# Optimization experiments

Measured on AMD Instinct MI355X. Metric: run time of the kernel, lower is better.

Reference implementation:

```python
import jax, jax.numpy as jnp
import numpy as np

BN_EPS = 1e-5
DIST_EPS = 1e-8


def setup_inputs() -> dict:
    key = jax.random.key(0)
    ks = jax.random.split(key, 10)
    B, Ni, Mi = 4, 16384, 4096
    C1, C2 = 64, 64
    Cin = C1 + C2  # 128, mlp=[128,128,128]
    inp = {
        "unknown": jax.random.normal(ks[0], (B * Ni, 3), dtype=jnp.float32),
        "unknown_batch_cnt": np.full(B, Ni, dtype=np.int64),
        "known": jax.random.normal(ks[1], (B * Mi, 3), dtype=jnp.float32),
        "known_batch_cnt": np.full(B, Mi, dtype=np.int64),
        "unknown_feats": jax.random.normal(ks[2], (B * Ni, C1), dtype=jnp.float32),
        "known_feats": jax.random.normal(ks[3], (B * Mi, C2), dtype=jnp.float32),
        "W1": jax.random.normal(ks[4], (128, Cin), dtype=jnp.float32) * 0.05,
        "g1": jnp.ones((128,), dtype=jnp.float32),
        "b1": jnp.zeros((128,), dtype=jnp.float32),
        "W2": jax.random.normal(ks[5], (128, 128), dtype=jnp.float32) * 0.05,
        "g2": jnp.ones((128,), dtype=jnp.float32),
        "b2": jnp.zeros((128,), dtype=jnp.float32),
    }
    return inp


def _three_nn(u, k):
    # u: (B,Ni,3), k: (B,Mi,3) -> dist (B,Ni,3), idx (B,Ni,3) within each batch
    d2 = (jnp.sum(u * u, -1)[:, :, None] + jnp.sum(k * k, -1)[:, None, :]
          - 2.0 * jnp.einsum("bnd,bmd->bnm", u, k))  # (B,Ni,Mi)
    neg_d2, idx = jax.lax.top_k(-d2, 3)
    dist = jnp.sqrt(jnp.maximum(-neg_d2, 0.0))
    return dist, idx


def _bn_relu(y, g, b):
    # BatchNorm2d over the point dim (training-mode batch stats), then ReLU
    mu = jnp.mean(y, axis=0)
    var = jnp.mean((y - mu) ** 2, axis=0)
    return jax.nn.relu((y - mu) * jax.lax.rsqrt(var + BN_EPS) * g + b)


def reference(unknown, unknown_batch_cnt, known, known_batch_cnt,
              unknown_feats, known_feats, W1, g1, b1, W2, g2, b2):
    ucnt = np.asarray(unknown_batch_cnt)
    kcnt = np.asarray(known_batch_cnt)
    B = ucnt.shape[0]
    Ni, Mi = int(ucnt[0]), int(kcnt[0])  # equal-count ragged batches
    C2 = known_feats.shape[1]

    u = unknown.reshape(B, Ni, 3)
    k = known.reshape(B, Mi, 3)
    dist, idx = _three_nn(u, k)

    dist_recip = 1.0 / (dist + DIST_EPS)
    weight = dist_recip / jnp.sum(dist_recip, axis=-1, keepdims=True)  # (B,Ni,3)

    kf = known_feats.reshape(B, Mi, C2)
    gathered = kf[jnp.arange(B)[:, None, None], idx]  # (B,Ni,3,C2)
    interp = jnp.sum(weight[..., None] * gathered, axis=2).reshape(B * Ni, C2)

    x = jnp.concatenate([interp, unknown_feats], axis=1)  # (N, C2+C1)
    x = _bn_relu(x @ W1.T, g1, b1)
    x = _bn_relu(x @ W2.T, g2, b2)
    return x
```

## Files before the change

### kernel.cpp

```cpp
#include <hip/hip_runtime.h>
#include <hip/hip_bf16.h>

#define GRID  32
#define NCELL (GRID * GRID * GRID)
#define H     0.3125f
#define INVH  3.2f
#define OFF   5.0f
#define SUBW  8
#define XPAD  136
#define NREP  16

using f32x4  = __attribute__((ext_vector_type(4))) float;
using bf16x8 = __attribute__((ext_vector_type(8))) short;

static __device__ inline short f2bs(float f) {
  __hip_bfloat16 h = __float2bfloat16(f);
  return __builtin_bit_cast(short, h);
}
static __device__ inline float bs2f(short s) {
  return __bfloat162float(__builtin_bit_cast(__hip_bfloat16, s));
}
static __device__ inline int cellco(float x) {
  int c = (int)((x + OFF) * INVH);
  return min(GRID - 1, max(0, c));
}

#define INSF(dv, mv)                                   \
  {                                                    \
    bool q0 = dv < b0, q1 = dv < b1, q2 = dv < b2;     \
    float P0 = b0, P1 = b1; int Q0 = j0, Q1 = j1;      \
    b2 = q1 ? P1 : (q2 ? dv : b2);                     \
    j2 = q1 ? Q1 : (q2 ? mv : j2);                     \
    b1 = q0 ? P0 : (q1 ? dv : P1);                     \
    j1 = q0 ? Q0 : (q1 ? mv : Q1);                     \
    b0 = q0 ? dv : P0;                                 \
    j0 = q0 ? mv : Q0;                                 \
  }

#define MERGE3(lo_mk, hi_mk)                                                        \
  for (int mk = lo_mk; mk <= hi_mk; mk <<= 1) {                                     \
    float ob0 = __shfl_xor(b0, mk), ob1 = __shfl_xor(b1, mk), ob2 = __shfl_xor(b2, mk); \
    int   oj0 = __shfl_xor(j0, mk), oj1 = __shfl_xor(j1, mk), oj2 = __shfl_xor(j2, mk); \
    INSF(ob0, oj0); INSF(ob1, oj1); INSF(ob2, oj2);                                 \
  }

__global__ __launch_bounds__(256) void zero_k(int4* __restrict__ dst, int n4) {
  int i = blockIdx.x * 256 + threadIdx.x;
  if (i < n4) dst[i] = int4{0, 0, 0, 0};
}

__global__ __launch_bounds__(256) void hist_k(
    const float* __restrict__ known, int Mtot, int Mi,
    const float* __restrict__ unknown, int Ntot,
    int* __restrict__ khist, int* __restrict__ qhist,
    int* __restrict__ kcell, int* __restrict__ qcell,
    const float* __restrict__ W1, const float* __restrict__ W2,
    __hip_bfloat16* __restrict__ Wb1, __hip_bfloat16* __restrict__ Wb2) {
  int i = blockIdx.x * 256 + threadIdx.x;
  if (i < 128 * 128) {
    Wb1[i] = __float2bfloat16(W1[i]);
    Wb2[i] = __float2bfloat16(W2[i]);
  }
  if (i < Mtot) {
    int b = i / Mi;
    float x = known[(size_t)i * 3], y = known[(size_t)i * 3 + 1], z = known[(size_t)i * 3 + 2];
    int c = b * NCELL + (cellco(z) * GRID + cellco(y)) * GRID + cellco(x);
    kcell[i] = c;
    atomicAdd(&khist[c], 1);
  }
  if (i < Ntot) {
    int Ni = Ntot / (Mtot / Mi);
    int b = i / Ni;
    float x = unknown[(size_t)i * 3], y = unknown[(size_t)i * 3 + 1], z = unknown[(size_t)i * 3 + 2];
    int c = b * NCELL + (cellco(z) * GRID + cellco(y)) * GRID + cellco(x);
    qcell[i] = c;
    atomicAdd(&qhist[c], 1);
  }
}

__global__ __launch_bounds__(256) void scan1_k(
    const int4* __restrict__ Hc4, int* __restrict__ bsum) {
  __shared__ int sh[256];
  int t = threadIdx.x;
  int4 h = Hc4[blockIdx.x * 256 + t];
  int s = h.x + h.y + h.z + h.w;
  sh[t] = s;
  __syncthreads();
  for (int d = 128; d > 0; d >>= 1) {
    if (t < d) sh[t] += sh[t + d];
    __syncthreads();
  }
  if (t == 0) bsum[blockIdx.x] = sh[0];
}

__global__ __launch_bounds__(256) void scan2_k(
    int* __restrict__ bsum, int nb, int* __restrict__ kstart, int* __restrict__ qstart,
    int nc, int Mtot, int Ntot) {
  __shared__ int sh[256];
  int t = threadIdx.x;
  int v = (t < nb) ? bsum[t] : 0;
  sh[t] = v;
  __syncthreads();
  for (int d = 1; d < 256; d <<= 1) {
    int u = (t >= d) ? sh[t - d] : 0;
    __syncthreads();
    sh[t] += u;
    __syncthreads();
  }
  if (t < nb) bsum[t] = sh[t] - v;
  if (t == 0) { kstart[nc] = Mtot; qstart[nc] = Ntot; }
}

__global__ __launch_bounds__(256) void scan3_k(
    const int4* __restrict__ Hc4, const int* __restrict__ bsum,
    int* __restrict__ kstart, int* __restrict__ kfill,
    int* __restrict__ qstart, int* __restrict__ qfill, int nc, int Mtot) {
  __shared__ int sh[256];
  int t = threadIdx.x;
  int g4 = blockIdx.x * 256 + t;
  int4 h = Hc4[g4];
  int s = h.x + h.y + h.z + h.w;
  sh[t] = s;
  __syncthreads();
  for (int d = 1; d < 256; d <<= 1) {
    int u = (t >= d) ? sh[t - d] : 0;
    __syncthreads();
    sh[t] += u;
    __syncthreads();
  }
  int run = bsum[blockIdx.x] + sh[t] - s;
  int hv[4] = {h.x, h.y, h.z, h.w};
#pragma unroll
  for (int j = 0; j < 4; ++j) {
    int g = g4 * 4 + j;
    if (g < nc) { kstart[g] = run; kfill[g] = run; }
    else        { int q = g - nc; qstart[q] = run - Mtot; qfill[q] = run - Mtot; }
    run += hv[j];
  }
}

__global__ __launch_bounds__(256) void scatter_k(
    const float* __restrict__ known, int Mtot, int Mi,
    const float* __restrict__ unknown, int Ntot,
    const int* __restrict__ kcell, const int* __restrict__ qcell,
    int* __restrict__ kfill, int* __restrict__ qfill,
    f32x4* __restrict__ k4s, int* __restrict__ korder,
    f32x4* __restrict__ u4s, int* __restrict__ qorder) {
  int i = blockIdx.x * 256 + threadIdx.x;
  if (i < Mtot) {
    int slot = atomicAdd(&kfill[kcell[i]], 1);
    float x = known[(size_t)i * 3], y = known[(size_t)i * 3 + 1], z = known[(size_t)i * 3 + 2];
    f32x4 v;
    v[0] = -2.f * x; v[1] = -2.f * y; v[2] = -2.f * z;
    v[3] = x * x + y * y + z * z;
    k4s[slot] = v;
    korder[slot] = i - (i / Mi) * Mi;
  }
  if (i < Ntot) {
    int slot = atomicAdd(&qfill[qcell[i]], 1);
    float x = unknown[(size_t)i * 3], y = unknown[(size_t)i * 3 + 1], z = unknown[(size_t)i * 3 + 2];
    f32x4 v;
    v[0] = x; v[1] = y; v[2] = z;
    v[3] = __fmaf_rn(x, x, __fmaf_rn(y, y, z * z));
    u4s[slot] = v;
    qorder[slot] = i;
  }
}

static __device__ __forceinline__ void scan_box_strided(
    int R, int sub, int stride, int cx, int cy, int cz, int cellbase,
    const int* __restrict__ cstart, const f32x4* __restrict__ k4s,
    const int* __restrict__ korder,
    float ux, float uy, float uz,
    float& b0, float& b1, float& b2, int& j0, int& j1, int& j2) {
  int zlo = max(cz - R, 0), zhi = min(cz + R, GRID - 1);
  int ylo = max(cy - R, 0), yhi = min(cy + R, GRID - 1);
  int xlo = max(cx - R, 0), xhi = min(cx + R, GRID - 1);
  int ny = yhi - ylo + 1;
  int nrows = (zhi - zlo + 1) * ny;
  for (int rid = sub; rid < nrows; rid += stride) {
    int zz = rid / ny;
    int y  = ylo + (rid - zz * ny);
    int row = cellbase + ((zlo + zz) * GRID + y) * GRID;
    int s = cstart[row + xlo];
    int e = cstart[row + xhi + 1];
    for (int i = s; i < e; ++i) {
      f32x4 k = k4s[i];
      float d = __fmaf_rn(ux, k[0], __fmaf_rn(uy, k[1], __fmaf_rn(uz, k[2], k[3])));
      int m = korder[i];
      INSF(d, m);
    }
  }
}

__global__ __launch_bounds__(256) void knn_grid_k(
    const f32x4* __restrict__ u4s, const int* __restrict__ qorder,
    const int* __restrict__ cstart, const f32x4* __restrict__ k4s,
    const int* __restrict__ korder, int Ni,
    float* __restrict__ w, int* __restrict__ idx,
    int* __restrict__ rcnt, int* __restrict__ rlist, float* __restrict__ rd3) {
  int nwc = gridDim.x * 4;
  int gw  = blockIdx.x * 4 + (threadIdx.x >> 6);
  int wchunk = (gw * 997) & (nwc - 1);
  int s   = wchunk * 8 + ((threadIdx.x & 63) / SUBW);
  int sub = threadIdx.x & (SUBW - 1);
  f32x4 u4 = u4s[s];
  int p = qorder[s];
  int b = p / Ni;
  float ux = u4[0], uy = u4[1], uz = u4[2], uu = u4[3];
  int cx = cellco(ux), cy = cellco(uy), cz = cellco(uz);
  int cellbase = b * NCELL;
  int xlo = max(cx - 1, 0), xhi = min(cx + 1, GRID - 1);

  float b0 = 3e38f, b1 = 3e38f, b2 = 3e38f;
  int   j0 = 0,     j1 = 0,     j2 = 0;
#pragma unroll
  for (int dz = -1; dz <= 1; ++dz) {
    int z = cz + dz;
    if (z < 0 || z >= GRID) continue;
#pragma unroll
    for (int dy = -1; dy <= 1; ++dy) {
      int y = cy + dy;
      if (y < 0 || y >= GRID) continue;
      int row = cellbase + (z * GRID + y) * GRID;
      int cs = cstart[row + xlo];
      int ce = cstart[row + xhi + 1];
      for (int i = cs + sub; i < ce; i += SUBW) {
        f32x4 k = k4s[i];
        float d = __fmaf_rn(ux, k[0], __fmaf_rn(uy, k[1], __fmaf_rn(uz, k[2], k[3])));
        int m = korder[i];
        INSF(d, m);
      }
    }
  }
  MERGE3(1, SUBW / 2);

  float d3sq = b2 + uu;
  bool ok = d3sq <= H * H;

  if (sub == 0) {
    if (ok) {
      float d0 = sqrtf(fmaxf(b0 + uu, 0.f));
      float d1 = sqrtf(fmaxf(b1 + uu, 0.f));
      float d2 = sqrtf(fmaxf(b2 + uu, 0.f));
      float r0 = 1.f / (d0 + 1e-8f);
      float r1 = 1.f / (d1 + 1e-8f);
      float r2 = 1.f / (d2 + 1e-8f);
      float rs = 1.f / (r0 + r1 + r2);
      size_t o = (size_t)p * 3;
      w[o] = r0 * rs; w[o + 1] = r1 * rs; w[o + 2] = r2 * rs;
      idx[o] = j0; idx[o + 1] = j1; idx[o + 2] = j2;
    } else {
      int t = atomicAdd(rcnt, 1);
      rlist[t] = s;
      rd3[t] = d3sq;
    }
  }
}

__global__ __launch_bounds__(256) void knn_retry_k(
    const f32x4* __restrict__ u4s, const int* __restrict__ qorder,
    const int* __restrict__ rlist, const float* __restrict__ rd3,
    const int* __restrict__ rcnt,
    const int* __restrict__ cstart, const f32x4* __restrict__ k4s,
    const int* __restrict__ korder, int Ni,
    float* __restrict__ w, int* __restrict__ idx) {
  int lane = threadIdx.x & 63;
  int wv   = blockIdx.x * 4 + (threadIdx.x >> 6);
  int nw   = gridDim.x * 4;
  int cnt  = rcnt[0];
  for (int q = wv; q < cnt; q += nw) {
    int sq = rlist[q];
    f32x4 u4 = u4s[sq];
    int p = qorder[sq];
    int b = p / Ni;
    float ux = u4[0], uy = u4[1], uz = u4[2], uu = u4[3];
    int cx = cellco(ux), cy = cellco(uy), cz = cellco(uz);
    int cellbase = b * NCELL;

    float d3sq = rd3[q];
    int Rc = 1;
    float b0, b1, b2; int j0, j1, j2;
    bool ok = false;
    while (!ok) {
      if (d3sq < 1e30f) {
        Rc = max((int)ceilf(sqrtf(fmaxf(d3sq, 0.f)) * INVH), Rc + 1);
      } else {
        Rc = Rc * 2;
      }
      Rc = min(Rc, GRID);
      b0 = b1 = b2 = 3e38f; j0 = j1 = j2 = 0;
      scan_box_strided(Rc, lane, 64, cx, cy, cz, cellbase, cstart, k4s, korder,
                       ux, uy, uz, b0, b1, b2, j0, j1, j2);
      MERGE3(1, 32);
      d3sq = b2 + uu;
      float cov = (float)Rc * H;
      ok = (d3sq <= cov * cov) || (Rc >= GRID);
    }
    if (lane == 0) {
      float d0 = sqrtf(fmaxf(b0 + uu, 0.f));
      float d1 = sqrtf(fmaxf(b1 + uu, 0.f));
      float d2 = sqrtf(fmaxf(b2 + uu, 0.f));
      float r0 = 1.f / (d0 + 1e-8f);
      float r1 = 1.f / (d1 + 1e-8f);
      float r2 = 1.f / (d2 + 1e-8f);
      float rs = 1.f / (r0 + r1 + r2);
      size_t o = (size_t)p * 3;
      w[o] = r0 * rs; w[o + 1] = r1 * rs; w[o + 2] = r2 * rs;
      idx[o] = j0; idx[o + 1] = j1; idx[o + 2] = j2;
    }
  }
}

template <bool F32OUT>
static __device__ __forceinline__ void gemm_half(
    const short* xs, const short* Ws, int row0,
    float* yf, __hip_bfloat16* yb, float* ls, float* lq) {
  int t = threadIdx.x;
  int lane = t & 63;
  int wv = t >> 6;
  int r = lane & 15, g = lane >> 4;
  int tile = wv >> 1, half = wv & 1;
  int trow = tile * 16;

  bf16x8 a[4];
#pragma unroll
  for (int q = 0; q < 4; ++q)
    a[q] = *reinterpret_cast<const bf16x8*>(&xs[(trow + r) * XPAD + g * 8 + q * 32]);

  int orow = row0 + trow + g * 4;
#pragma unroll
  for (int ct = 0; ct < 4; ++ct) {
    int ocol = half * 64 + ct * 16 + r;
    f32x4 acc = {0.f, 0.f, 0.f, 0.f};
    size_t bbase = (size_t)ocol * 128 + g * 8;
#pragma unroll
    for (int q = 0; q < 4; ++q) {
      bf16x8 bfr = *reinterpret_cast<const bf16x8*>(Ws + bbase + q * 32);
      acc = __builtin_amdgcn_mfma_f32_16x16x32_bf16(a[q], bfr, acc, 0, 0, 0);
    }
    if (F32OUT) {
#pragma unroll
      for (int i = 0; i < 4; ++i)
        yf[(size_t)(orow + i) * 128 + ocol] = acc[i];
    } else {
#pragma unroll
      for (int i = 0; i < 4; ++i)
        yb[(size_t)(orow + i) * 128 + ocol] = __float2bfloat16(acc[i]);
    }
    float s  = acc[0] + acc[1] + acc[2] + acc[3];
    float q2 = acc[0] * acc[0] + acc[1] * acc[1] + acc[2] * acc[2] + acc[3] * acc[3];
    s  += __shfl_xor(s, 16);  s  += __shfl_xor(s, 32);
    q2 += __shfl_xor(q2, 16); q2 += __shfl_xor(q2, 32);
    if (g == 0) {
      atomicAdd(&ls[ocol], s);
      atomicAdd(&lq[ocol], q2);
    }
  }
}

__global__ __launch_bounds__(256) void gemm1_fused_k(
    const float* __restrict__ kf, const float* __restrict__ uf,
    const float* __restrict__ wgt, const int* __restrict__ idx,
    const __hip_bfloat16* __restrict__ Wb, __hip_bfloat16* __restrict__ Yb,
    float* __restrict__ stats, int Ni, int Mi) {
  __shared__ short xs[32 * XPAD];
  __shared__ float ls[128], lq[128];
  int t = threadIdx.x;
  if (t < 128) { ls[t] = 0.f; lq[t] = 0.f; }
  int row0 = blockIdx.x * 32;

  int rr = t >> 3, c0 = (t & 7) * 16;
  int p = row0 + rr;
  short tmp[16];
  if (c0 < 64) {
    size_t o = (size_t)p * 3;
    float w0 = wgt[o], w1 = wgt[o + 1], w2 = wgt[o + 2];
    int i0 = idx[o], i1 = idx[o + 1], i2 = idx[o + 2];
    int b = p / Ni;
    const float* kfb = kf + (size_t)b * Mi * 64 + c0;
    const f32x4* r0p = reinterpret_cast<const f32x4*>(kfb + (size_t)i0 * 64);
    const f32x4* r1p = reinterpret_cast<const f32x4*>(kfb + (size_t)i1 * 64);
    const f32x4* r2p = reinterpret_cast<const f32x4*>(kfb + (size_t)i2 * 64);
#pragma unroll
    for (int j = 0; j < 4; ++j) {
      f32x4 av = r0p[j], bv = r1p[j], cv = r2p[j];
#pragma unroll
      for (int e = 0; e < 4; ++e)
        tmp[j * 4 + e] = f2bs(w0 * av[e] + w1 * bv[e] + w2 * cv[e]);
    }
  } else {
    const f32x4* ufp = reinterpret_cast<const f32x4*>(uf + (size_t)p * 64 + (c0 - 64));
#pragma unroll
    for (int j = 0; j < 4; ++j) {
      f32x4 av = ufp[j];
#pragma unroll
      for (int e = 0; e < 4; ++e)
        tmp[j * 4 + e] = f2bs(av[e]);
    }
  }
  *reinterpret_cast<bf16x8*>(&xs[rr * XPAD + c0])     = *reinterpret_cast<bf16x8*>(&tmp[0]);
  *reinterpret_cast<bf16x8*>(&xs[rr * XPAD + c0 + 8]) = *reinterpret_cast<bf16x8*>(&tmp[8]);
  __syncthreads();

  gemm_half<false>(xs, reinterpret_cast<const short*>(Wb), row0, nullptr, Yb, ls, lq);

  __syncthreads();
  if (t < 128) {
    int rep = blockIdx.x & (NREP - 1);
    atomicAdd(&stats[rep * 256 + t], ls[t]);
    atomicAdd(&stats[rep * 256 + 128 + t], lq[t]);
  }
}

__global__ __launch_bounds__(256) void gemm2_bn_k(
    const __hip_bfloat16* __restrict__ Y1, const float* __restrict__ AB,
    const __hip_bfloat16* __restrict__ Wb, float* __restrict__ Yf,
    float* __restrict__ stats) {
  __shared__ short xs[32 * XPAD];
  __shared__ float ls[128], lq[128];
  int t = threadIdx.x;
  if (t < 128) { ls[t] = 0.f; lq[t] = 0.f; }
  int row0 = blockIdx.x * 32;

  int rr = t >> 3, c0 = (t & 7) * 16;
  int p = row0 + rr;
  const short* Ys = reinterpret_cast<const short*>(Y1);
  bf16x8 v0 = *reinterpret_cast<const bf16x8*>(Ys + (size_t)p * 128 + c0);
  bf16x8 v1 = *reinterpret_cast<const bf16x8*>(Ys + (size_t)p * 128 + c0 + 8);
  short tmp[16];
#pragma unroll
  for (int j = 0; j < 8; ++j)
    tmp[j] = f2bs(fmaxf(bs2f(v0[j]) * AB[c0 + j] + AB[128 + c0 + j], 0.f));
#pragma unroll
  for (int j = 0; j < 8; ++j)
    tmp[8 + j] = f2bs(fmaxf(bs2f(v1[j]) * AB[c0 + 8 + j] + AB[128 + c0 + 8 + j], 0.f));
  *reinterpret_cast<bf16x8*>(&xs[rr * XPAD + c0])     = *reinterpret_cast<bf16x8*>(&tmp[0]);
  *reinterpret_cast<bf16x8*>(&xs[rr * XPAD + c0 + 8]) = *reinterpret_cast<bf16x8*>(&tmp[8]);
  __syncthreads();

  gemm_half<true>(xs, reinterpret_cast<const short*>(Wb), row0, Yf, nullptr, ls, lq);

  __syncthreads();
  if (t < 128) {
    int rep = blockIdx.x & (NREP - 1);
    atomicAdd(&stats[rep * 256 + t], ls[t]);
    atomicAdd(&stats[rep * 256 + 128 + t], lq[t]);
  }
}

__global__ void finalize_k(const float* __restrict__ stats, const float* __restrict__ g,
                           const float* __restrict__ bb, float invN, float* __restrict__ AB) {
  int c = threadIdx.x;
  float s = 0.f, q = 0.f;
  for (int rpl = 0; rpl < NREP; ++rpl) {
    s += stats[rpl * 256 + c];
    q += stats[rpl * 256 + 128 + c];
  }
  float mu  = s * invN;
  float var = q * invN - mu * mu;
  float A = rsqrtf(var + 1e-5f) * g[c];
  AB[c] = A;
  AB[128 + c] = bb[c] - mu * A;
}

__global__ __launch_bounds__(256) void bnrelu_f32_k(
    float* __restrict__ Y, const float* __restrict__ AB, long n4) {
  long i = (long)blockIdx.x * 256 + threadIdx.x;
  long stride = (long)gridDim.x * 256;
  for (; i < n4; i += stride) {
    f32x4 y = reinterpret_cast<f32x4*>(Y)[i];
    int c0 = (int)((i * 4) & 127);
    f32x4 A  = *reinterpret_cast<const f32x4*>(AB + c0);
    f32x4 Bv = *reinterpret_cast<const f32x4*>(AB + 128 + c0);
    f32x4 o;
#pragma unroll
    for (int j = 0; j < 4; ++j) o[j] = fmaxf(y[j] * A[j] + Bv[j], 0.f);
    reinterpret_cast<f32x4*>(Y)[i] = o;
  }
}

extern "C" void kernel_launch(void* const* d_in, const int* in_sizes, int n_in,
                              void* d_out, int out_size, void* d_ws, size_t ws_size,
                              hipStream_t stream) {
  const float* unknown = (const float*)d_in[0];
  const float* known   = (const float*)d_in[2];
  const float* uf      = (const float*)d_in[4];
  const float* kf      = (const float*)d_in[5];
  const float* W1      = (const float*)d_in[6];
  const float* g1      = (const float*)d_in[7];
  const float* b1      = (const float*)d_in[8];
  const float* W2      = (const float*)d_in[9];
  const float* g2      = (const float*)d_in[10];
  const float* b2      = (const float*)d_in[11];

  int B    = in_sizes[1];
  int Ntot = in_sizes[0] / 3;
  int Mtot = in_sizes[2] / 3;
  int Ni = Ntot / B, Mi = Mtot / B;
  int nc = B * NCELL;
  int n2 = 2 * nc;

  char* ws = (char*)d_ws;
  size_t off = 0;
  auto alloc = [&](size_t bytes) {
    void* p = ws + off;
    off += (bytes + 255) & ~(size_t)255;
    return p;
  };
  float* stats  = (float*)alloc(2 * NREP * 256 * 4);
  int*   rcnt   = (int*)alloc(4);
  int*   khist  = (int*)alloc((size_t)n2 * 4);
  int*   qhist  = khist + nc;
  size_t zero_bytes = (size_t)((char*)(khist + n2) - (char*)stats);
  int*   kstart = (int*)alloc((size_t)(nc + 1) * 4);
  int*   qstart = (int*)alloc((size_t)(nc + 1) * 4);
  int*   kfill  = (int*)alloc((size_t)nc * 4);
  int*   qfill  = (int*)alloc((size_t)nc * 4);
  int*   kcell  = (int*)alloc((size_t)Mtot * 4);
  int*   qcell  = (int*)alloc((size_t)Ntot * 4);
  int*   korder = (int*)alloc((size_t)Mtot * 4);
  int*   qorder = (int*)alloc((size_t)Ntot * 4);
  int*   bsum   = (int*)alloc((size_t)(n2 / 1024) * 4);
  int*   rlist  = (int*)alloc((size_t)Ntot * 4);
  float* rd3    = (float*)alloc((size_t)Ntot * 4);
  f32x4* k4s    = (f32x4*)alloc((size_t)Mtot * 16);
  f32x4* u4s    = (f32x4*)alloc((size_t)Ntot * 16);
  float* wgt    = (float*)alloc((size_t)Ntot * 3 * 4);
  int*   idx    = (int*)alloc((size_t)Ntot * 3 * 4);
  __hip_bfloat16* y1b = (__hip_bfloat16*)alloc((size_t)Ntot * 128 * 2);
  __hip_bfloat16* Wb1 = (__hip_bfloat16*)alloc(128 * 128 * 2);
  __hip_bfloat16* Wb2 = (__hip_bfloat16*)alloc(128 * 128 * 2);
  float* AB1 = (float*)alloc(256 * 4);
  float* AB2 = (float*)alloc(256 * 4);

  float* y2 = (float*)d_out;
  long n4 = (long)Ntot * 128 / 4;
  float invN = 1.0f / (float)Ntot;
  int nb = n2 / 1024;
  float* stats2 = stats + NREP * 256;
  int zn4 = (int)(zero_bytes / 16);

  zero_k<<<(zn4 + 255) / 256, 256, 0, stream>>>((int4*)stats, zn4);
  hist_k<<<(Ntot + 255) / 256, 256, 0, stream>>>(known, Mtot, Mi, unknown, Ntot,
                                                 khist, qhist, kcell, qcell, W1, W2, Wb1, Wb2);
  scan1_k<<<nb, 256, 0, stream>>>((const int4*)khist, bsum);
  scan2_k<<<1, 256, 0, stream>>>(bsum, nb, kstart, qstart, nc, Mtot, Ntot);
  scan3_k<<<nb, 256, 0, stream>>>((const int4*)khist, bsum, kstart, kfill, qstart, qfill, nc, Mtot);
  scatter_k<<<(Ntot + 255) / 256, 256, 0, stream>>>(known, Mtot, Mi, unknown, Ntot,
                                                    kcell, qcell, kfill, qfill, k4s, korder, u4s, qorder);
  knn_grid_k<<<Ntot / 32, 256, 0, stream>>>(u4s, qorder, kstart, k4s, korder, Ni,
                                            wgt, idx, rcnt, rlist, rd3);
  knn_retry_k<<<1024, 256, 0, stream>>>(u4s, qorder, rlist, rd3, rcnt,
                                        kstart, k4s, korder, Ni, wgt, idx);
  gemm1_fused_k<<<Ntot / 32, 256, 0, stream>>>(kf, uf, wgt, idx, Wb1, y1b, stats, Ni, Mi);
  finalize_k<<<1, 128, 0, stream>>>(stats, g1, b1, invN, AB1);
  gemm2_bn_k<<<Ntot / 32, 256, 0, stream>>>(y1b, AB1, Wb2, y2, stats2);
  finalize_k<<<1, 128, 0, stream>>>(stats2, g2, b2, invN, AB2);
  bnrelu_f32_k<<<2048, 256, 0, stream>>>(y2, AB2, n4);
}
```

Baseline: 161.4 us.

## Fuse both MLP layers and BN passes into one persistent kernel with grid barriers

New measurement: 394.6 us. +144.5%, slower.

```diff
diff --git a/kernel.cpp b/kernel.cpp
--- a/kernel.cpp
+++ b/kernel.cpp
@@ -16,9 +16,6 @@
 static __device__ inline short f2bs(float f) {
   __hip_bfloat16 h = __float2bfloat16(f);
   return __builtin_bit_cast(short, h);
-}
-static __device__ inline float bs2f(short s) {
-  return __bfloat162float(__builtin_bit_cast(__hip_bfloat16, s));
 }
 static __device__ inline int cellco(float x) {
   int c = (int)((x + OFF) * INVH);
@@ -312,44 +309,56 @@
   }
 }
 
-template <bool F32OUT>
-static __device__ __forceinline__ void gemm_half(
-    const short* xs, const short* Ws, int row0,
-    float* yf, __hip_bfloat16* yb, float* ls, float* lq) {
-  int t = threadIdx.x;
-  int lane = t & 63;
-  int wv = t >> 6;
-  int r = lane & 15, g = lane >> 4;
-  int tile = wv >> 1, half = wv & 1;
-  int trow = tile * 16;
-
+
+static __device__ __forceinline__ void grid_bar(int* bar, int target) {
+  __syncthreads();
+  if (threadIdx.x == 0) {
+    __threadfence();
+    __hip_atomic_fetch_add(bar, 1, __ATOMIC_ACQ_REL, __HIP_MEMORY_SCOPE_AGENT);
+    while (__hip_atomic_load(bar, __ATOMIC_ACQUIRE, __HIP_MEMORY_SCOPE_AGENT) < target) {}
+  }
+  __syncthreads();
+}
+
+#define TGEOM                                  \
+  int t = threadIdx.x;                         \
+  int lane = t & 63;                           \
+  int wv = t >> 6;                             \
+  int r = lane & 15, g = lane >> 4;            \
+  int wtile = wv >> 1, half = wv & 1;          \
+  int trow = wtile * 16;
+
+static __device__ __forceinline__ void gemm_tile(
+    const short* xs, const short* Ws, f32x4 acc[4]) {
+  TGEOM
+  (void)wtile;
   bf16x8 a[4];
 #pragma unroll
   for (int q = 0; q < 4; ++q)
     a[q] = *reinterpret_cast<const bf16x8*>(&xs[(trow + r) * XPAD + g * 8 + q * 32]);
-
-  int orow = row0 + trow + g * 4;
 #pragma unroll
   for (int ct = 0; ct < 4; ++ct) {
     int ocol = half * 64 + ct * 16 + r;
-    f32x4 acc = {0.f, 0.f, 0.f, 0.f};
+    f32x4 v = {0.f, 0.f, 0.f, 0.f};
     size_t bbase = (size_t)ocol * 128 + g * 8;
 #pragma unroll
     for (int q = 0; q < 4; ++q) {
       bf16x8 bfr = *reinterpret_cast<const bf16x8*>(Ws + bbase + q * 32);
-      acc = __builtin_amdgcn_mfma_f32_16x16x32_bf16(a[q], bfr, acc, 0, 0, 0);
-    }
-    if (F32OUT) {
-#pragma unroll
-      for (int i = 0; i < 4; ++i)
-        yf[(size_t)(orow + i) * 128 + ocol] = acc[i];
-    } else {
-#pragma unroll
-      for (int i = 0; i < 4; ++i)
-        yb[(size_t)(orow + i) * 128 + ocol] = __float2bfloat16(acc[i]);
-    }
-    float s  = acc[0] + acc[1] + acc[2] + acc[3];
-    float q2 = acc[0] * acc[0] + acc[1] * acc[1] + acc[2] * acc[2] + acc[3] * acc[3];
+      v = __builtin_amdgcn_mfma_f32_16x16x32_bf16(a[q], bfr, v, 0, 0, 0);
+    }
+    acc[ct] = v;
+  }
+}
+
+static __device__ __forceinline__ void acc_stats(const f32x4 acc[4], float* ls, float* lq) {
+  TGEOM
+  (void)wtile; (void)trow;
+#pragma unroll
+  for (int ct = 0; ct < 4; ++ct) {
+    int ocol = half * 64 + ct * 16 + r;
+    float s  = acc[ct][0] + acc[ct][1] + acc[ct][2] + acc[ct][3];
+    float q2 = acc[ct][0] * acc[ct][0] + acc[ct][1] * acc[ct][1]
+             + acc[ct][2] * acc[ct][2] + acc[ct][3] * acc[ct][3];
     s  += __shfl_xor(s, 16);  s  += __shfl_xor(s, 32);
     q2 += __shfl_xor(q2, 16); q2 += __shfl_xor(q2, 32);
     if (g == 0) {
@@ -359,124 +368,142 @@
   }
 }
 
-__global__ __launch_bounds__(256) void gemm1_fused_k(
+__global__ __launch_bounds__(256, 4) void mlp_fused_k(
     const float* __restrict__ kf, const float* __restrict__ uf,
     const float* __restrict__ wgt, const int* __restrict__ idx,
-    const __hip_bfloat16* __restrict__ Wb, __hip_bfloat16* __restrict__ Yb,
-    float* __restrict__ stats, int Ni, int Mi) {
+    const __hip_bfloat16* __restrict__ Wb1, const __hip_bfloat16* __restrict__ Wb2,
+    const float* __restrict__ g1, const float* __restrict__ b1v,
+    const float* __restrict__ g2, const float* __restrict__ b2v,
+    float* __restrict__ stats, int* __restrict__ bar,
+    float* __restrict__ y2, int Ni, int Mi, float invN, int nblocks) {
   __shared__ short xs[32 * XPAD];
   __shared__ float ls[128], lq[128];
-  int t = threadIdx.x;
+  __shared__ float ABs[256];
+  TGEOM
+  const short* W1s = reinterpret_cast<const short*>(Wb1);
+  const short* W2s = reinterpret_cast<const short*>(Wb2);
+  float* stats2 = stats + NREP * 256;
+  int rep = blockIdx.x & (NREP - 1);
+  int srow = t >> 3, c0 = (t & 7) * 16;
+
   if (t < 128) { ls[t] = 0.f; lq[t] = 0.f; }
-  int row0 = blockIdx.x * 32;
-
-  int rr = t >> 3, c0 = (t & 7) * 16;
-  int p = row0 + rr;
-  short tmp[16];
-  if (c0 < 64) {
-    size_t o = (size_t)p * 3;
-    float w0 = wgt[o], w1 = wgt[o + 1], w2 = wgt[o + 2];
-    int i0 = idx[o], i1 = idx[o + 1], i2 = idx[o + 2];
-    int b = p / Ni;
-    const float* kfb = kf + (size_t)b * Mi * 64 + c0;
-    const f32x4* r0p = reinterpret_cast<const f32x4*>(kfb + (size_t)i0 * 64);
-    const f32x4* r1p = reinterpret_cast<const f32x4*>(kfb + (size_t)i1 * 64);
-    const f32x4* r2p = reinterpret_cast<const f32x4*>(kfb + (size_t)i2 * 64);
-#pragma unroll
-    for (int j = 0; j < 4; ++j) {
-      f32x4 av = r0p[j], bv = r1p[j], cv = r2p[j];
-#pragma unroll
-      for (int e = 0; e < 4; ++e)
-        tmp[j * 4 + e] = f2bs(w0 * av[e] + w1 * bv[e] + w2 * cv[e]);
-    }
-  } else {
-    const f32x4* ufp = reinterpret_cast<const f32x4*>(uf + (size_t)p * 64 + (c0 - 64));
-#pragma unroll
-    for (int j = 0; j < 4; ++j) {
-      f32x4 av = ufp[j];
-#pragma unroll
-      for (int e = 0; e < 4; ++e)
-        tmp[j * 4 + e] = f2bs(av[e]);
-    }
-  }
-  *reinterpret_cast<bf16x8*>(&xs[rr * XPAD + c0])     = *reinterpret_cast<bf16x8*>(&tmp[0]);
-  *reinterpret_cast<bf16x8*>(&xs[rr * XPAD + c0 + 8]) = *reinterpret_cast<bf16x8*>(&tmp[8]);
-  __syncthreads();
-
-  gemm_half<false>(xs, reinterpret_cast<const short*>(Wb), row0, nullptr, Yb, ls, lq);
-
-  __syncthreads();
+  __syncthreads();
+
+  f32x4 acc1[2][4];
+#pragma unroll 2
+  for (int tt = 0; tt < 2; ++tt) {
+    int row0 = (blockIdx.x * 2 + tt) * 32;
+    int p = row0 + srow;
+    short tmp[16];
+    if (c0 < 64) {
+      size_t o = (size_t)p * 3;
+      float w0 = wgt[o], w1 = wgt[o + 1], w2 = wgt[o + 2];
+      int i0 = idx[o], i1 = idx[o + 1], i2 = idx[o + 2];
+      int b = p / Ni;
+      const float* kfb = kf + (size_t)b * Mi * 64 + c0;
+      const f32x4* r0p = reinterpret_cast<const f32x4*>(kfb + (size_t)i0 * 64);
+      const f32x4* r1p = reinterpret_cast<const f32x4*>(kfb + (size_t)i1 * 64);
+      const f32x4* r2p = reinterpret_cast<const f32x4*>(kfb + (size_t)i2 * 64);
+#pragma unroll
+      for (int j = 0; j < 4; ++j) {
+        f32x4 av = r0p[j], bv = r1p[j], cv = r2p[j];
+#pragma unroll
+        for (int e = 0; e < 4; ++e)
+          tmp[j * 4 + e] = f2bs(w0 * av[e] + w1 * bv[e] + w2 * cv[e]);
+      }
+    } else {
+      const f32x4* ufp = reinterpret_cast<const f32x4*>(uf + (size_t)p * 64 + (c0 - 64));
+#pragma unroll
+      for (int j = 0; j < 4; ++j) {
+        f32x4 av = ufp[j];
+#pragma unroll
+        for (int e = 0; e < 4; ++e)
+          tmp[j * 4 + e] = f2bs(av[e]);
+      }
+    }
+    *reinterpret_cast<bf16x8*>(&xs[srow * XPAD + c0])     = *reinterpret_cast<bf16x8*>(&tmp[0]);
+    *reinterpret_cast<bf16x8*>(&xs[srow * XPAD + c0 + 8]) = *reinterpret_cast<bf16x8*>(&tmp[8]);
+    __syncthreads();
+    if (tt == 0) { gemm_tile(xs, W1s, acc1[0]); acc_stats(acc1[0], ls, lq); }
+    else         { gemm_tile(xs, W1s, acc1[1]); acc_stats(acc1[1], ls, lq); }
+    __syncthreads();
+  }
   if (t < 128) {
-    int rep = blockIdx.x & (NREP - 1);
     atomicAdd(&stats[rep * 256 + t], ls[t]);
     atomicAdd(&stats[rep * 256 + 128 + t], lq[t]);
   }
-}
-
-__global__ __launch_bounds__(256) void gemm2_bn_k(
-    const __hip_bfloat16* __restrict__ Y1, const float* __restrict__ AB,
-    const __hip_bfloat16* __restrict__ Wb, float* __restrict__ Yf,
-    float* __restrict__ stats) {
-  __shared__ short xs[32 * XPAD];
-  __shared__ float ls[128], lq[128];
-  int t = threadIdx.x;
-  if (t < 128) { ls[t] = 0.f; lq[t] = 0.f; }
-  int row0 = blockIdx.x * 32;
-
-  int rr = t >> 3, c0 = (t & 7) * 16;
-  int p = row0 + rr;
-  const short* Ys = reinterpret_cast<const short*>(Y1);
-  bf16x8 v0 = *reinterpret_cast<const bf16x8*>(Ys + (size_t)p * 128 + c0);
-  bf16x8 v1 = *reinterpret_cast<const bf16x8*>(Ys + (size_t)p * 128 + c0 + 8);
-  short tmp[16];
-#pragma unroll
-  for (int j = 0; j < 8; ++j)
-    tmp[j] = f2bs(fmaxf(bs2f(v0[j]) * AB[c0 + j] + AB[128 + c0 + j], 0.f));
-#pragma unroll
-  for (int j = 0; j < 8; ++j)
-    tmp[8 + j] = f2bs(fmaxf(bs2f(v1[j]) * AB[c0 + 8 + j] + AB[128 + c0 + 8 + j], 0.f));
-  *reinterpret_cast<bf16x8*>(&xs[rr * XPAD + c0])     = *reinterpret_cast<bf16x8*>(&tmp[0]);
-  *reinterpret_cast<bf16x8*>(&xs[rr * XPAD + c0 + 8]) = *reinterpret_cast<bf16x8*>(&tmp[8]);
-  __syncthreads();
-
-  gemm_half<true>(xs, reinterpret_cast<const short*>(Wb), row0, Yf, nullptr, ls, lq);
-
-  __syncthreads();
+
+  grid_bar(bar, nblocks);
+
   if (t < 128) {
-    int rep = blockIdx.x & (NREP - 1);
-    atomicAdd(&stats[rep * 256 + t], ls[t]);
-    atomicAdd(&stats[rep * 256 + 128 + t], lq[t]);
-  }
-}
-
-__global__ void finalize_k(const float* __restrict__ stats, const float* __restrict__ g,
-                           const float* __restrict__ bb, float invN, float* __restrict__ AB) {
-  int c = threadIdx.x;
-  float s = 0.f, q = 0.f;
-  for (int rpl = 0; rpl < NREP; ++rpl) {
-    s += stats[rpl * 256 + c];
-    q += stats[rpl * 256 + 128 + c];
-  }
-  float mu  = s * invN;
-  float var = q * invN - mu * mu;
-  float A = rsqrtf(var + 1e-5f) * g[c];
-  AB[c] = A;
-  AB[128 + c] = bb[c] - mu * A;
-}
-
-__global__ __launch_bounds__(256) void bnrelu_f32_k(
-    float* __restrict__ Y, const float* __restrict__ AB, long n4) {
-  long i = (long)blockIdx.x * 256 + threadIdx.x;
-  long stride = (long)gridDim.x * 256;
-  for (; i < n4; i += stride) {
-    f32x4 y = reinterpret_cast<f32x4*>(Y)[i];
-    int c0 = (int)((i * 4) & 127);
-    f32x4 A  = *reinterpret_cast<const f32x4*>(AB + c0);
-    f32x4 Bv = *reinterpret_cast<const f32x4*>(AB + 128 + c0);
-    f32x4 o;
-#pragma unroll
-    for (int j = 0; j < 4; ++j) o[j] = fmaxf(y[j] * A[j] + Bv[j], 0.f);
-    reinterpret_cast<f32x4*>(Y)[i] = o;
+    float s = 0.f, q = 0.f;
+#pragma unroll
+    for (int rpl = 0; rpl < NREP; ++rpl) {
+      s += __hip_atomic_load(&stats[rpl * 256 + t], __ATOMIC_RELAXED, __HIP_MEMORY_SCOPE_AGENT);
+      q += __hip_atomic_load(&stats[rpl * 256 + 128 + t], __ATOMIC_RELAXED, __HIP_MEMORY_SCOPE_AGENT);
+    }
+    float mu  = s * invN;
+    float var = q * invN - mu * mu;
+    float A = rsqrtf(var + 1e-5f) * g1[t];
+    ABs[t] = A;
+    ABs[128 + t] = b1v[t] - mu * A;
+    ls[t] = 0.f; lq[t] = 0.f;
+  }
+  __syncthreads();
+
+  f32x4 acc2[2][4];
+#pragma unroll 2
+  for (int tt = 0; tt < 2; ++tt) {
+#pragma unroll
+    for (int ct = 0; ct < 4; ++ct) {
+      int ocol = half * 64 + ct * 16 + r;
+      float A = ABs[ocol], Bv = ABs[128 + ocol];
+#pragma unroll
+      for (int i = 0; i < 4; ++i) {
+        float v = fmaxf((tt == 0 ? acc1[0][ct][i] : acc1[1][ct][i]) * A + Bv, 0.f);
+        xs[(trow + g * 4 + i) * XPAD + ocol] = f2bs(v);
+      }
+    }
+    __syncthreads();
+    if (tt == 0) { gemm_tile(xs, W2s, acc2[0]); acc_stats(acc2[0], ls, lq); }
+    else         { gemm_tile(xs, W2s, acc2[1]); acc_stats(acc2[1], ls, lq); }
+    __syncthreads();
+  }
+  if (t < 128) {
+    atomicAdd(&stats2[rep * 256 + t], ls[t]);
+    atomicAdd(&stats2[rep * 256 + 128 + t], lq[t]);
+  }
+
+  grid_bar(bar, 2 * nblocks);
+
+  if (t < 128) {
+    float s = 0.f, q = 0.f;
+#pragma unroll
+    for (int rpl = 0; rpl < NREP; ++rpl) {
+      s += __hip_atomic_load(&stats2[rpl * 256 + t], __ATOMIC_RELAXED, __HIP_MEMORY_SCOPE_AGENT);
+      q += __hip_atomic_load(&stats2[rpl * 256 + 128 + t], __ATOMIC_RELAXED, __HIP_MEMORY_SCOPE_AGENT);
+    }
+    float mu  = s * invN;
+    float var = q * invN - mu * mu;
+    float A = rsqrtf(var + 1e-5f) * g2[t];
+    ABs[t] = A;
+    ABs[128 + t] = b2v[t] - mu * A;
+  }
+  __syncthreads();
+
+#pragma unroll 2
+  for (int tt = 0; tt < 2; ++tt) {
+    int row0 = (blockIdx.x * 2 + tt) * 32;
+#pragma unroll
+    for (int ct = 0; ct < 4; ++ct) {
+      int ocol = half * 64 + ct * 16 + r;
+      float A = ABs[ocol], Bv = ABs[128 + ocol];
+#pragma unroll
+      for (int i = 0; i < 4; ++i) {
+        float v = fmaxf((tt == 0 ? acc2[0][ct][i] : acc2[1][ct][i]) * A + Bv, 0.f);
+        y2[(size_t)(row0 + trow + g * 4 + i) * 128 + ocol] = v;
+      }
+    }
   }
 }
 
@@ -509,7 +536,8 @@
     return p;
   };
   float* stats  = (float*)alloc(2 * NREP * 256 * 4);
-  int*   rcnt   = (int*)alloc(4);
+  int*   rcnt   = (int*)alloc(8);
+  int*   bar    = rcnt + 1;
   int*   khist  = (int*)alloc((size_t)n2 * 4);
   int*   qhist  = khist + nc;
   size_t zero_bytes = (size_t)((char*)(khist + n2) - (char*)stats);
@@ -528,18 +556,14 @@
   f32x4* u4s    = (f32x4*)alloc((size_t)Ntot * 16);
   float* wgt    = (float*)alloc((size_t)Ntot * 3 * 4);
   int*   idx    = (int*)alloc((size_t)Ntot * 3 * 4);
-  __hip_bfloat16* y1b = (__hip_bfloat16*)alloc((size_t)Ntot * 128 * 2);
   __hip_bfloat16* Wb1 = (__hip_bfloat16*)alloc(128 * 128 * 2);
   __hip_bfloat16* Wb2 = (__hip_bfloat16*)alloc(128 * 128 * 2);
-  float* AB1 = (float*)alloc(256 * 4);
-  float* AB2 = (float*)alloc(256 * 4);
 
   float* y2 = (float*)d_out;
-  long n4 = (long)Ntot * 128 / 4;
   float invN = 1.0f / (float)Ntot;
   int nb = n2 / 1024;
-  float* stats2 = stats + NREP * 256;
   int zn4 = (int)(zero_bytes / 16);
+  int nblocks = Ntot / 64;
 
   zero_k<<<(zn4 + 255) / 256, 256, 0, stream>>>((int4*)stats, zn4);
   hist_k<<<(Ntot + 255) / 256, 256, 0, stream>>>(known, Mtot, Mi, unknown, Ntot,
@@ -553,9 +577,7 @@
                                             wgt, idx, rcnt, rlist, rd3);
   knn_retry_k<<<1024, 256, 0, stream>>>(u4s, qorder, rlist, rd3, rcnt,
                                         kstart, k4s, korder, Ni, wgt, idx);
-  gemm1_fused_k<<<Ntot / 32, 256, 0, stream>>>(kf, uf, wgt, idx, Wb1, y1b, stats, Ni, Mi);
-  finalize_k<<<1, 128, 0, stream>>>(stats, g1, b1, invN, AB1);
-  gemm2_bn_k<<<Ntot / 32, 256, 0, stream>>>(y1b, AB1, Wb2, y2, stats2);
-  finalize_k<<<1, 128, 0, stream>>>(stats2, g2, b2, invN, AB2);
-  bnrelu_f32_k<<<2048, 256, 0, stream>>>(y2, AB2, n4);
-}
+  mlp_fused_k<<<nblocks, 256, 0, stream>>>(kf, uf, wgt, idx, Wb1, Wb2,
+                                           g1, b1, g2, b2, stats, bar, y2,
+                                           Ni, Mi, invN, nblocks);
+}
```
